# Performance work log

Hardware: AMD Instinct MI355X
Metric: run time of the kernel (lower is better)

## Reference

```python
import jax, jax.numpy as jnp
import numpy as np

M_FACTORS = [12, 8, 8]
N_FACTORS = [8, 8, 12]
E = 4          # hardcoded in original: gates.view(B, 4, 1, 1, 1)
R = 8          # TT rank
ALPHA = 16.0   # common_alpha
TAU = 1.0


def setup_inputs() -> dict:
    key = jax.random.key(0)
    ks = jax.random.split(key, 11)
    B, S, m = 32, 512, 768
    inp = {
        "X": jax.random.normal(ks[0], (B, S, m), jnp.float32),
        "router_w": jax.random.normal(ks[1], (E, m), jnp.float32) * 0.02,
        "router_b": jax.random.normal(ks[2], (E,), jnp.float32) * 0.02,
        "base_w": jax.random.normal(ks[3], (m, m), jnp.float32) * 0.02,
        "base_b": jax.random.normal(ks[4], (m,), jnp.float32) * 0.02,
        "core0": jax.random.normal(ks[5], (E, 1, 12, R), jnp.float32) * 0.1,
        "core1": jax.random.normal(ks[6], (E, R, 8, R), jnp.float32) * 0.1,
        "core2": jax.random.normal(ks[7], (E, R, 8, R), jnp.float32) * 0.1,
        "core3": jax.random.normal(ks[8], (E, R, 8, R), jnp.float32) * 0.1,
        "core4": jax.random.normal(ks[9], (E, R, 8, R), jnp.float32) * 0.1,
        "core5": jax.random.normal(ks[10], (E, R, 12, 1), jnp.float32) * 0.1,
    }
    return inp


def _gumbel_softmax_hard(logits, key):
    # torch.nn.functional.gumbel_softmax(logits, tau=TAU, hard=True)
    u = jax.random.uniform(key, logits.shape, logits.dtype, 1e-6, 1.0 - 1e-6)
    g = -jnp.log(-jnp.log(u))
    y_soft = jax.nn.softmax((logits + g) / TAU, axis=-1)
    y_hard = jax.nn.one_hot(jnp.argmax(y_soft, axis=-1), logits.shape[-1],
                            dtype=logits.dtype)
    # straight-through: y_hard - sg(y_soft) + y_soft
    return jax.lax.stop_gradient(y_hard - y_soft) + y_soft


def _tt_moe(X, gates, cores):
    # faithful to tensorized_multiplication_experts
    B, S, m = X.shape
    # [B, 1, S, m_factors[::-1]] -> last axis is m_factors[0]
    tt_state = X.reshape([B, 1, S] + M_FACTORS[::-1])
    num_m = len(M_FACTORS)
    for i in range(num_m):
        # per-sample expert-weighted core: [B, r, f, p]
        mc = jnp.einsum('be,erfp->brfp', gates, cores[i])
        tt_state = jnp.einsum('br...m,brmp->bp...', tt_state, mc)
    for i in range(len(N_FACTORS)):
        mc = jnp.einsum('be,erfp->brfp', gates, cores[num_m + i])
        tt_state = jnp.einsum('br...,brnp->bp...n', tt_state, mc)
    return tt_state.reshape(B, S, -1)  # trailing p == 1


def reference(X, router_w, router_b, base_w, base_b,
              core0, core1, core2, core3, core4, core5):
    cores = [core0, core1, core2, core3, core4, core5]
    pooled = X.mean(axis=1)                              # [B, m]
    logits = pooled @ router_w.T + router_b              # [B, E]
    gates = _gumbel_softmax_hard(logits, jax.random.key(42))
    base_out = X @ base_w.T + base_b                     # F.linear
    Z = _tt_moe(X, gates, cores)                         # [B, S, n]
    return Z * ALPHA + base_out
```

## Files before the change

kernel.cpp:

```cpp
#include <hip/hip_runtime.h>
#include <hip/hip_bf16.h>
#include <stdint.h>

#define GAS __attribute__((address_space(1)))
#define LAS __attribute__((address_space(3)))

typedef __attribute__((ext_vector_type(8))) short bf16x8;
typedef __attribute__((ext_vector_type(4))) float f32x4;

struct us4 { unsigned short x, y, z, w; };

__device__ __forceinline__ void gl_lds16(const void* g, void* lds) {
  __builtin_amdgcn_global_load_lds((const GAS unsigned int*)(uintptr_t)g,
                                   (LAS unsigned int*)(uintptr_t)lds, 16, 0, 0);
}

__device__ __forceinline__ unsigned short f2bf(float f) {
  unsigned u = __float_as_uint(f);
  return (unsigned short)((u + 0x7fffu + ((u >> 16) & 1u)) >> 16);
}

__device__ __forceinline__ void threefry2x32_42(unsigned x0, unsigned x1,
                                                unsigned* o0, unsigned* o1) {
  const unsigned k0 = 0u, k1 = 42u;
  unsigned ks[3] = {k0, k1, k0 ^ k1 ^ 0x1BD11BDAu};
  x0 += ks[0]; x1 += ks[1];
  const int rot[2][4] = {{13, 15, 26, 6}, {17, 29, 16, 24}};
#pragma unroll
  for (int i = 0; i < 5; ++i) {
#pragma unroll
    for (int j = 0; j < 4; ++j) {
      int r = rot[i & 1][j];
      x0 += x1;
      x1 = (x1 << r) | (x1 >> (32 - r));
      x1 ^= x0;
    }
    x0 += ks[(i + 1) % 3];
    x1 += ks[(i + 2) % 3] + (unsigned)(i + 1);
  }
  *o0 = x0; *o1 = x1;
}

__global__ __launch_bounds__(256) void k_prep(
    const float* __restrict__ X, const float* __restrict__ rw,
    const float* __restrict__ bw,
    const float* __restrict__ c0, const float* __restrict__ c1,
    const float* __restrict__ c2, const float* __restrict__ c3,
    const float* __restrict__ c4, const float* __restrict__ c5,
    unsigned short* __restrict__ Xbf, float* __restrict__ partial,
    unsigned short* __restrict__ Wbt) {
  __shared__ __align__(16) char smem[31232];
  int t = threadIdx.x;
  int bid = blockIdx.x;

  if (bid < 192) {
    int e = bid / 48, jc = bid % 48;
    float* KA = (float*)smem;
    float* LB = (float*)(smem + 3072);
    float* Kt = (float*)(smem + 6144);
    float* LtS = (float*)(smem + 30720);
    for (int q = t; q < 768; q += 256) {
      int bc = q >> 3, p2 = q & 7;
      int b2 = bc / 12, cc = bc % 12;
      float s = 0.f;
#pragma unroll
      for (int p1 = 0; p1 < 8; ++p1)
        s += c0[e * 96 + cc * 8 + p1] * c1[((e * 8 + p1) * 8 + b2) * 8 + p2];
      KA[q] = s;
      int p4 = q / 96, mm = q % 96;
      int n2 = mm / 12, n3 = mm % 12;
      float s2 = 0.f;
#pragma unroll
      for (int p5 = 0; p5 < 8; ++p5)
        s2 += c4[((e * 8 + p4) * 8 + n2) * 8 + p5] * c5[(e * 8 + p5) * 12 + n3];
      LB[q] = s2;
    }
    __syncthreads();
    for (int q = t; q < 6144; q += 256) {
      int i = q >> 3, p3 = q & 7;
      int a = i / 96, bc = i % 96;
      float s = 0.f;
#pragma unroll
      for (int p2 = 0; p2 < 8; ++p2)
        s += KA[bc * 8 + p2] * c2[((e * 8 + p2) * 8 + a) * 8 + p3];
      Kt[p3 * 768 + i] = s;
    }
    if (t < 128) {
      int i = t >> 3, p3 = t & 7;
      int j = jc * 16 + i;
      int n1 = j / 96, mm = j % 96;
      float s2 = 0.f;
#pragma unroll
      for (int p4 = 0; p4 < 8; ++p4)
        s2 += c3[((e * 8 + p3) * 8 + n1) * 8 + p4] * LB[p4 * 96 + mm];
      LtS[i * 8 + p3] = s2;
    }
    __syncthreads();
    for (int idx = t; idx < 12288; idx += 256) {
      int jl = idx / 768, i = idx - jl * 768;
      int j = jc * 16 + jl;
      float s = 0.f;
#pragma unroll
      for (int p = 0; p < 8; ++p) s += Kt[p * 768 + i] * LtS[jl * 8 + p];
      float val = bw[(size_t)j * 768 + i] + 16.0f * s;
      Wbt[(size_t)e * 589824 + (size_t)j * 768 + i] = f2bf(val);
    }
  } else {
    float* red = (float*)smem;
    int p = bid - 192;
    int r0 = p * 32;
    float lp0 = 0.f, lp1 = 0.f, lp2 = 0.f, lp3 = 0.f;
    if (t < 192) {
      const float* xp = X + (size_t)r0 * 768 + t * 4;
      unsigned short* xo = Xbf + (size_t)r0 * 768 + t * 4;
      float4 acc = {0.f, 0.f, 0.f, 0.f};
#pragma unroll 8
      for (int r = 0; r < 32; ++r) {
        float4 v = *reinterpret_cast<const float4*>(xp + (size_t)r * 768);
        acc.x += v.x; acc.y += v.y; acc.z += v.z; acc.w += v.w;
        us4 o;
        o.x = f2bf(v.x); o.y = f2bf(v.y); o.z = f2bf(v.z); o.w = f2bf(v.w);
        *reinterpret_cast<us4*>(xo + (size_t)r * 768) = o;
      }
      float4 w0 = *reinterpret_cast<const float4*>(rw + 0 * 768 + t * 4);
      float4 w1 = *reinterpret_cast<const float4*>(rw + 1 * 768 + t * 4);
      float4 w2 = *reinterpret_cast<const float4*>(rw + 2 * 768 + t * 4);
      float4 w3 = *reinterpret_cast<const float4*>(rw + 3 * 768 + t * 4);
      lp0 = acc.x * w0.x + acc.y * w0.y + acc.z * w0.z + acc.w * w0.w;
      lp1 = acc.x * w1.x + acc.y * w1.y + acc.z * w1.z + acc.w * w1.w;
      lp2 = acc.x * w2.x + acc.y * w2.y + acc.z * w2.z + acc.w * w2.w;
      lp3 = acc.x * w3.x + acc.y * w3.y + acc.z * w3.z + acc.w * w3.w;
    }
#pragma unroll
    for (int off = 32; off > 0; off >>= 1) {
      lp0 += __shfl_down(lp0, off);
      lp1 += __shfl_down(lp1, off);
      lp2 += __shfl_down(lp2, off);
      lp3 += __shfl_down(lp3, off);
    }
    int w = t >> 6;
    if ((t & 63) == 0 && w < 3) {
      red[w * 4 + 0] = lp0; red[w * 4 + 1] = lp1;
      red[w * 4 + 2] = lp2; red[w * 4 + 3] = lp3;
    }
    __syncthreads();
    if (t < 4) partial[p * 4 + t] = red[0 + t] + red[4 + t] + red[8 + t];
  }
}

__global__ __launch_bounds__(256, 4) void k_gemm(
    const unsigned short* __restrict__ Xbf,
    const unsigned short* __restrict__ Wbt,
    const float* __restrict__ partial,
    const float* __restrict__ rb,
    const float* __restrict__ base_b,
    float* __restrict__ out)
{
  __shared__ unsigned short sA[128 * 64];
  __shared__ unsigned short sB[128 * 64];
  __shared__ int sExp;
  int t = threadIdx.x;
  int w = t >> 6, l = t & 63;
  int l16 = l & 15, l4 = l >> 4;

  int bid = blockIdx.x;
  int work = (bid & 7) * 96 + (bid >> 3);
  int mtile = work / 6, ntile = work - mtile * 6;
  int m0 = mtile * 128, n0 = ntile * 128;
  int b = mtile >> 2;

  if (t < 4) {
    float s = 0.f;
#pragma unroll
    for (int c = 0; c < 16; ++c) s += partial[(b * 16 + c) * 4 + t];
    float lg = s * (1.0f / 512.0f) + rb[t];
    int idx = b * 4 + t;
    unsigned x0, x1;
    threefry2x32_42(0u, (unsigned)idx, &x0, &x1);
    unsigned bits = x0 ^ x1;
    float u01 = __uint_as_float((bits >> 9) | 0x3f800000u) - 1.0f;
    float u = u01 * ((1.0f - 1e-6f) - 1e-6f) + 1e-6f;
    u = fmaxf(u, 1e-6f);
    float v = lg + (-logf(-logf(u)));
    int bi = t;
#pragma unroll
    for (int off = 1; off < 4; off <<= 1) {
      float vo = __shfl_xor(v, off);
      int io = __shfl_xor(bi, off);
      if (vo > v || (vo == v && io < bi)) { v = vo; bi = io; }
    }
    if (t == 0) sExp = bi;
  }
  __syncthreads();
  int e = sExp;
  const unsigned short* Wb = Wbt + (size_t)e * 589824;
  int wr = w >> 1, wc = w & 1;

  f32x4 acc[4][4];
#pragma unroll
  for (int i = 0; i < 4; ++i)
#pragma unroll
    for (int jj = 0; jj < 4; ++jj) acc[i][jj] = (f32x4)0.f;

  int rows[4], csw[4];
#pragma unroll
  for (int q = 0; q < 4; ++q) {
    int ci = (w * 4 + q) * 64 + l;
    rows[q] = ci >> 3;
    csw[q] = ((ci & 7) * 8) ^ ((rows[q] & 7) << 3);
  }

  int xorr = (l16 & 7) << 3;
  for (int k0 = 0; k0 < 768; k0 += 64) {
#pragma unroll
    for (int q = 0; q < 4; ++q) {
      const unsigned short* ga = Xbf + (size_t)(m0 + rows[q]) * 768 + k0 + csw[q];
      gl_lds16(ga, &sA[(w * 4 + q) * 512]);
      const unsigned short* gb = Wb + (size_t)(n0 + rows[q]) * 768 + k0 + csw[q];
      gl_lds16(gb, &sB[(w * 4 + q) * 512]);
    }
    __syncthreads();
#pragma unroll
    for (int kk = 0; kk < 2; ++kk) {
      int coff = (kk * 32 + l4 * 8) ^ xorr;
      bf16x8 af[4], bfr[4];
#pragma unroll
      for (int am = 0; am < 4; ++am)
        af[am] = *reinterpret_cast<const bf16x8*>(
            &sA[(wr * 64 + am * 16 + l16) * 64 + coff]);
#pragma unroll
      for (int bn = 0; bn < 4; ++bn)
        bfr[bn] = *reinterpret_cast<const bf16x8*>(
            &sB[(wc * 64 + bn * 16 + l16) * 64 + coff]);
#pragma unroll
      for (int am = 0; am < 4; ++am)
#pragma unroll
        for (int bn = 0; bn < 4; ++bn)
          acc[am][bn] = __builtin_amdgcn_mfma_f32_16x16x32_bf16(
              bfr[bn], af[am], acc[am][bn], 0, 0, 0);
    }
    __syncthreads();
  }

  f32x4 bb4[4];
#pragma unroll
  for (int bn = 0; bn < 4; ++bn)
    bb4[bn] = *reinterpret_cast<const f32x4*>(base_b + n0 + wc * 64 + bn * 16 + l4 * 4);
#pragma unroll
  for (int am = 0; am < 4; ++am) {
    int m = m0 + wr * 64 + am * 16 + l16;
    float* op = out + (size_t)m * 768 + n0 + wc * 64 + l4 * 4;
#pragma unroll
    for (int bn = 0; bn < 4; ++bn) {
      f32x4 v = acc[am][bn] + bb4[bn];
      __builtin_nontemporal_store(v, reinterpret_cast<f32x4*>(op + bn * 16));
    }
  }
}

extern "C" void kernel_launch(void* const* d_in, const int* in_sizes, int n_in,
                              void* d_out, int out_size, void* d_ws, size_t ws_size,
                              hipStream_t stream) {
  const float* X  = (const float*)d_in[0];
  const float* rw = (const float*)d_in[1];
  const float* rb = (const float*)d_in[2];
  const float* bw = (const float*)d_in[3];
  const float* bb = (const float*)d_in[4];
  const float* c0 = (const float*)d_in[5];
  const float* c1 = (const float*)d_in[6];
  const float* c2 = (const float*)d_in[7];
  const float* c3 = (const float*)d_in[8];
  const float* c4 = (const float*)d_in[9];
  const float* c5 = (const float*)d_in[10];
  float* out = (float*)d_out;

  char* ws = (char*)d_ws;
  float* partial      = (float*)(ws + 4096);
  unsigned short* Wbt = (unsigned short*)(ws + 262144);
  unsigned short* Xbf = (unsigned short*)(ws + 4980736);

  k_prep<<<704, 256, 0, stream>>>(X, rw, bw, c0, c1, c2, c3, c4, c5,
                                  Xbf, partial, Wbt);
  k_gemm<<<768, 256, 0, stream>>>(Xbf, Wbt, partial, rb, bb, out);
}
```

Measured before the change: 58.85 us.

## Double-buffer GEMM LDS tiles with K=32 stages and per-wave expert selection

```diff
diff --git a/kernel.cpp b/kernel.cpp
--- a/kernel.cpp
+++ b/kernel.cpp
@@ -156,9 +156,8 @@
     const float* __restrict__ base_b,
     float* __restrict__ out)
 {
-  __shared__ unsigned short sA[128 * 64];
-  __shared__ unsigned short sB[128 * 64];
-  __shared__ int sExp;
+  __shared__ unsigned short sA[2][4096];
+  __shared__ unsigned short sB[2][4096];
   int t = threadIdx.x;
   int w = t >> 6, l = t & 63;
   int l16 = l & 15, l4 = l >> 4;
@@ -169,78 +168,91 @@
   int m0 = mtile * 128, n0 = ntile * 128;
   int b = mtile >> 2;
 
-  if (t < 4) {
-    float s = 0.f;
-#pragma unroll
-    for (int c = 0; c < 16; ++c) s += partial[(b * 16 + c) * 4 + t];
-    float lg = s * (1.0f / 512.0f) + rb[t];
-    int idx = b * 4 + t;
-    unsigned x0, x1;
-    threefry2x32_42(0u, (unsigned)idx, &x0, &x1);
-    unsigned bits = x0 ^ x1;
-    float u01 = __uint_as_float((bits >> 9) | 0x3f800000u) - 1.0f;
-    float u = u01 * ((1.0f - 1e-6f) - 1e-6f) + 1e-6f;
-    u = fmaxf(u, 1e-6f);
-    float v = lg + (-logf(-logf(u)));
-    int bi = t;
-#pragma unroll
-    for (int off = 1; off < 4; off <<= 1) {
-      float vo = __shfl_xor(v, off);
-      int io = __shfl_xor(bi, off);
-      if (vo > v || (vo == v && io < bi)) { v = vo; bi = io; }
-    }
-    if (t == 0) sExp = bi;
-  }
+  int bi = 0;
+  {
+    float v = -1e30f;
+    if (l < 4) {
+      float s = 0.f;
+#pragma unroll
+      for (int c = 0; c < 16; ++c) s += partial[(b * 16 + c) * 4 + l];
+      float lg = s * (1.0f / 512.0f) + rb[l];
+      int idx = b * 4 + l;
+      unsigned x0, x1;
+      threefry2x32_42(0u, (unsigned)idx, &x0, &x1);
+      unsigned bits = x0 ^ x1;
+      float u01 = __uint_as_float((bits >> 9) | 0x3f800000u) - 1.0f;
+      float u = u01 * ((1.0f - 1e-6f) - 1e-6f) + 1e-6f;
+      u = fmaxf(u, 1e-6f);
+      v = lg + (-logf(-logf(u)));
+      bi = l;
+#pragma unroll
+      for (int off = 1; off < 4; off <<= 1) {
+        float vo = __shfl_xor(v, off);
+        int io = __shfl_xor(bi, off);
+        if (vo > v || (vo == v && io < bi)) { v = vo; bi = io; }
+      }
+    }
+    bi = __shfl(bi, 0);
+  }
+  const unsigned short* Wb = Wbt + (size_t)bi * 589824;
+  int wr = w >> 1, wc = w & 1;
+
+  f32x4 acc[4][4];
+#pragma unroll
+  for (int i = 0; i < 4; ++i)
+#pragma unroll
+    for (int jj = 0; jj < 4; ++jj) acc[i][jj] = (f32x4)0.f;
+
+  int rows[2], ksw[2];
+#pragma unroll
+  for (int q = 0; q < 2; ++q) {
+    int ci = (w * 2 + q) * 64 + l;
+    rows[q] = ci >> 2;
+    int slot = ci & 3;
+    ksw[q] = (slot ^ ((rows[q] >> 1) & 3)) * 8;
+  }
+
+#define STAGE(bufi, k0)                                                        \
+  {                                                                            \
+    _Pragma("unroll") for (int q = 0; q < 2; ++q) {                            \
+      int ci = (w * 2 + q) * 64 + l;                                           \
+      const unsigned short* ga =                                               \
+          Xbf + (size_t)(m0 + rows[q]) * 768 + (k0) + ksw[q];                  \
+      gl_lds16(ga, &sA[bufi][ci * 8]);                                         \
+      const unsigned short* gb =                                               \
+          Wb + (size_t)(n0 + rows[q]) * 768 + (k0) + ksw[q];                   \
+      gl_lds16(gb, &sB[bufi][ci * 8]);                                         \
+    }                                                                          \
+  }
+
+  STAGE(0, 0);
   __syncthreads();
-  int e = sExp;
-  const unsigned short* Wb = Wbt + (size_t)e * 589824;
-  int wr = w >> 1, wc = w & 1;
-
-  f32x4 acc[4][4];
-#pragma unroll
-  for (int i = 0; i < 4; ++i)
-#pragma unroll
-    for (int jj = 0; jj < 4; ++jj) acc[i][jj] = (f32x4)0.f;
-
-  int rows[4], csw[4];
-#pragma unroll
-  for (int q = 0; q < 4; ++q) {
-    int ci = (w * 4 + q) * 64 + l;
-    rows[q] = ci >> 3;
-    csw[q] = ((ci & 7) * 8) ^ ((rows[q] & 7) << 3);
-  }
-
-  int xorr = (l16 & 7) << 3;
-  for (int k0 = 0; k0 < 768; k0 += 64) {
-#pragma unroll
-    for (int q = 0; q < 4; ++q) {
-      const unsigned short* ga = Xbf + (size_t)(m0 + rows[q]) * 768 + k0 + csw[q];
-      gl_lds16(ga, &sA[(w * 4 + q) * 512]);
-      const unsigned short* gb = Wb + (size_t)(n0 + rows[q]) * 768 + k0 + csw[q];
-      gl_lds16(gb, &sB[(w * 4 + q) * 512]);
-    }
-    __syncthreads();
-#pragma unroll
-    for (int kk = 0; kk < 2; ++kk) {
-      int coff = (kk * 32 + l4 * 8) ^ xorr;
-      bf16x8 af[4], bfr[4];
-#pragma unroll
-      for (int am = 0; am < 4; ++am)
-        af[am] = *reinterpret_cast<const bf16x8*>(
-            &sA[(wr * 64 + am * 16 + l16) * 64 + coff]);
+
+  for (int kt = 0; kt < 24; ++kt) {
+    int cur = kt & 1;
+    if (kt < 23) STAGE(cur ^ 1, (kt + 1) * 32);
+    bf16x8 af[4], bfr[4];
+#pragma unroll
+    for (int am = 0; am < 4; ++am) {
+      int row = wr * 64 + am * 16 + l16;
+      int slot = l4 ^ ((row >> 1) & 3);
+      af[am] = *reinterpret_cast<const bf16x8*>(&sA[cur][row * 32 + slot * 8]);
+    }
+#pragma unroll
+    for (int bn = 0; bn < 4; ++bn) {
+      int row = wc * 64 + bn * 16 + l16;
+      int slot = l4 ^ ((row >> 1) & 3);
+      bfr[bn] = *reinterpret_cast<const bf16x8*>(&sB[cur][row * 32 + slot * 8]);
+    }
+#pragma unroll
+    for (int am = 0; am < 4; ++am)
 #pragma unroll
       for (int bn = 0; bn < 4; ++bn)
-        bfr[bn] = *reinterpret_cast<const bf16x8*>(
-            &sB[(wc * 64 + bn * 16 + l16) * 64 + coff]);
-#pragma unroll
-      for (int am = 0; am < 4; ++am)
-#pragma unroll
-        for (int bn = 0; bn < 4; ++bn)
-          acc[am][bn] = __builtin_amdgcn_mfma_f32_16x16x32_bf16(
-              bfr[bn], af[am], acc[am][bn], 0, 0, 0);
-    }
-    __syncthreads();
-  }
+        acc[am][bn] = __builtin_amdgcn_mfma_f32_16x16x32_bf16(
+            bfr[bn], af[am], acc[am][bn], 0, 0, 0);
+    __syncthreads();
+  }
+#undef STAGE
 
   f32x4 bb4[4];
 #pragma unroll
```

Measured after the change: 62.85 us. 6.8% more time.
